# Performance work log

Hardware: AMD Instinct MI355X
Metric: run time of the kernel (lower is better)

## Reference

```python
import jax, jax.numpy as jnp
import numpy as np

WINDOW = 5  # len_sort_window in the original module


def setup_inputs() -> dict:
    key = jax.random.key(0)
    k1, k2, k3 = jax.random.split(key, 3)
    B, L, D = 8, 4000, 512  # L divisible by WINDOW, D < L
    q = jax.random.normal(k1, (B, L, D), dtype=jnp.float32)
    k = jax.random.normal(k2, (B, L, D), dtype=jnp.float32)
    v = jax.random.normal(k3, (B, L, D), dtype=jnp.float32)
    return {"q": q, "k": k, "v": v}


def reference(q, k, v):
    # q, k are unused by the original forward.
    B, L, D = v.shape
    t = jnp.arange(L)          # sequence positions
    s = jnp.arange(D)          # per-feature cyclic shift amount (= feature index)
    # Shift feature i left by i: shifted[:, t, i] = v[:, (t + i) % L, i]
    idx_fwd = (t[:, None] + s[None, :]) % L            # [L, D]
    v_shift = jnp.take_along_axis(v, idx_fwd[None, :, :], axis=1)  # [B, L, D]
    # Sort within fixed non-overlapping windows of size WINDOW along the seq axis.
    v_sorted = jnp.sort(v_shift.reshape(B, L // WINDOW, WINDOW, D), axis=2)
    v_sorted = v_sorted.reshape(B, L, D)
    # Unshift feature i right by i: out[:, t, i] = v_sorted[:, (t - i) % L, i]
    idx_bwd = (t[:, None] - s[None, :]) % L            # [L, D]
    return jnp.take_along_axis(v_sorted, idx_bwd[None, :, :], axis=1)
```

## Files before the change

### kernel.cpp

```cpp
#include <hip/hip_runtime.h>


constexpr int L = 4000;
constexpr int D = 512;

__global__ __launch_bounds__(256)
void swd18_window_sort(const float* __restrict__ v, float* __restrict__ out) {
    const int i = blockIdx.y * 256 + threadIdx.x;
    const int w = blockIdx.x;
    const int b = blockIdx.z;

    const int r = i % 5;
    const int s = w * 5 + r;

    const float* __restrict__ vb = v + (size_t)b * (size_t)(L * D);
    float*       __restrict__ ob = out + (size_t)b * (size_t)(L * D);

    int t0 = s;
    int t1 = s + 1; if (t1 >= L) t1 -= L;
    int t2 = s + 2; if (t2 >= L) t2 -= L;
    int t3 = s + 3; if (t3 >= L) t3 -= L;
    int t4 = s + 4; if (t4 >= L) t4 -= L;

    float x0 = vb[t0 * D + i];
    float x1 = vb[t1 * D + i];
    float x2 = vb[t2 * D + i];
    float x3 = vb[t3 * D + i];
    float x4 = vb[t4 * D + i];

#define CE(a, b) { float lo_ = fminf(a, b); float hi_ = fmaxf(a, b); a = lo_; b = hi_; }
    CE(x0, x1) CE(x3, x4) CE(x2, x4) CE(x2, x3) CE(x1, x4)
    CE(x0, x3) CE(x0, x2) CE(x1, x3) CE(x1, x2)
#undef CE

    ob[t0 * D + i] = x0;
    ob[t1 * D + i] = x1;
    ob[t2 * D + i] = x2;
    ob[t3 * D + i] = x3;
    ob[t4 * D + i] = x4;
}

extern "C" void kernel_launch(void* const* d_in, const int* in_sizes, int n_in,
                              void* d_out, int out_size, void* d_ws, size_t ws_size,
                              hipStream_t stream) {
    const float* v = (const float*)d_in[2];
    float* out = (float*)d_out;

    const int B = in_sizes[2] / (L * D);

    dim3 grid(L / 5, D / 256, B);
    swd18_window_sort<<<grid, dim3(256), 0, stream>>>(v, out);
}
```

Baseline: 193.7 us.

## Stage row tiles with halo in LDS and sort windows from shared memory

Each block now loads a 48-row by 128-column tile (40 output rows plus a 4-row wrap-around halo) into LDS with float4 loads. It runs the 5-element sorting network on every window overlapping that tile, then writes the 40 owned rows back with float4 stores. This replaces per-thread scalar gathers at staggered row offsets with coalesced vector traffic. The cost is about 20% redundant halo reads and two block barriers.

```diff
diff --git a/kernel.cpp b/kernel.cpp
--- a/kernel.cpp
+++ b/kernel.cpp
@@ -3,41 +3,65 @@
 
 constexpr int L = 4000;
 constexpr int D = 512;
+constexpr int TROWS = 40;
+constexpr int RROWS = 48;
+constexpr int CCOLS = 128;
+constexpr int NTHREADS = 256;
 
-__global__ __launch_bounds__(256)
-void swd18_window_sort(const float* __restrict__ v, float* __restrict__ out) {
-    const int i = blockIdx.y * 256 + threadIdx.x;
-    const int w = blockIdx.x;
-    const int b = blockIdx.z;
+__global__ __launch_bounds__(NTHREADS)
+void swd18_tile_sort(const float* __restrict__ v, float* __restrict__ out) {
+    __shared__ float tile[RROWS * CCOLS];
 
-    const int r = i % 5;
-    const int s = w * 5 + r;
+    const int tid = threadIdx.x;
+    const int w   = blockIdx.x;
+    const int C0  = blockIdx.y * CCOLS;
+    const int b   = blockIdx.z;
+    const int R0  = w * TROWS;
 
-    const float* __restrict__ vb = v + (size_t)b * (size_t)(L * D);
-    float*       __restrict__ ob = out + (size_t)b * (size_t)(L * D);
+    const float* __restrict__ vb = v   + (size_t)b * (L * D) + C0;
+    float*       __restrict__ ob = out + (size_t)b * (L * D) + C0;
 
-    int t0 = s;
-    int t1 = s + 1; if (t1 >= L) t1 -= L;
-    int t2 = s + 2; if (t2 >= L) t2 -= L;
-    int t3 = s + 3; if (t3 >= L) t3 -= L;
-    int t4 = s + 4; if (t4 >= L) t4 -= L;
+    for (int idx = tid; idx < RROWS * (CCOLS / 4); idx += NTHREADS) {
+        int lr = idx >> 5;
+        int c4 = (idx & 31) << 2;
+        int g  = R0 - 4 + lr;
+        if (g < 0)  g += L;
+        if (g >= L) g -= L;
+        float4 val = *(const float4*)(vb + (size_t)g * D + c4);
+        *(float4*)(&tile[lr * CCOLS + c4]) = val;
+    }
+    __syncthreads();
 
-    float x0 = vb[t0 * D + i];
-    float x1 = vb[t1 * D + i];
-    float x2 = vb[t2 * D + i];
-    float x3 = vb[t3 * D + i];
-    float x4 = vb[t4 * D + i];
+    for (int id = tid; id < 9 * CCOLS; id += NTHREADS) {
+        int col = id & (CCOLS - 1);
+        int k   = id >> 7;
+        int r   = (C0 + col) % 5;
+        int ls  = r - 1 + 5 * k;
+        if (ls < 0) continue;
+        float* p = &tile[ls * CCOLS + col];
+        float x0 = p[0 * CCOLS];
+        float x1 = p[1 * CCOLS];
+        float x2 = p[2 * CCOLS];
+        float x3 = p[3 * CCOLS];
+        float x4 = p[4 * CCOLS];
+#define CE(a, b) { float lo_ = fminf(a, b); float hi_ = fmaxf(a, b); a = lo_; b = hi_; }
+        CE(x0, x1) CE(x3, x4) CE(x2, x4) CE(x2, x3) CE(x1, x4)
+        CE(x0, x3) CE(x0, x2) CE(x1, x3) CE(x1, x2)
+#undef CE
+        p[0 * CCOLS] = x0;
+        p[1 * CCOLS] = x1;
+        p[2 * CCOLS] = x2;
+        p[3 * CCOLS] = x3;
+        p[4 * CCOLS] = x4;
+    }
+    __syncthreads();
 
-#define CE(a, b) { float lo_ = fminf(a, b); float hi_ = fmaxf(a, b); a = lo_; b = hi_; }
-    CE(x0, x1) CE(x3, x4) CE(x2, x4) CE(x2, x3) CE(x1, x4)
-    CE(x0, x3) CE(x0, x2) CE(x1, x3) CE(x1, x2)
-#undef CE
-
-    ob[t0 * D + i] = x0;
-    ob[t1 * D + i] = x1;
-    ob[t2 * D + i] = x2;
-    ob[t3 * D + i] = x3;
-    ob[t4 * D + i] = x4;
+    for (int idx = tid; idx < TROWS * (CCOLS / 4); idx += NTHREADS) {
+        int lr = (idx >> 5) + 4;
+        int c4 = (idx & 31) << 2;
+        int g  = R0 + lr - 4;
+        *(float4*)(ob + (size_t)g * D + c4) = *(const float4*)(&tile[lr * CCOLS + c4]);
+    }
 }
 
 extern "C" void kernel_launch(void* const* d_in, const int* in_sizes, int n_in,
@@ -48,6 +72,6 @@
 
     const int B = in_sizes[2] / (L * D);
 
-    dim3 grid(L / 5, D / 256, B);
-    swd18_window_sort<<<grid, dim3(256), 0, stream>>>(v, out);
+    dim3 grid(L / TROWS, D / CCOLS, B);
+    swd18_tile_sort<<<grid, dim3(NTHREADS), 0, stream>>>(v, out);
 }
```

Measured after the change: 184.0 us. 1.05x faster.

## Stream row strips per thread with float4 loads and register-carried window state

Applied to the files above, without the earlier changes.

Replaces the one-thread-per-window scalar kernel with threads that each own four adjacent feature columns and walk a 50-row strip. Loads are float4 and are software-pipelined one 5-row group ahead. Each column's shifted sort windows straddle two row groups, so the previous group and the pending output fragments are kept in registers and stitched with selects. The goal is wider memory transactions and less per-thread overhead. The cost is higher register pressure, select-heavy code, and a halo re-read of the previous group at each strip boundary.

```diff
diff --git a/kernel.cpp b/kernel.cpp
--- a/kernel.cpp
+++ b/kernel.cpp
@@ -3,42 +3,95 @@
 
 constexpr int L = 4000;
 constexpr int D = 512;
+constexpr int S = 50;
+constexpr int NSTRIPS = L / S;
+constexpr int NCG = D / 4;
 
-__global__ __launch_bounds__(256)
-void swd18_window_sort(const float* __restrict__ v, float* __restrict__ out) {
-    const int i = blockIdx.y * 256 + threadIdx.x;
-    const int w = blockIdx.x;
-    const int b = blockIdx.z;
+#define CE(a, b) { float lo_ = fminf(a, b); float hi_ = fmaxf(a, b); (a) = lo_; (b) = hi_; }
 
-    const int r = i % 5;
-    const int s = w * 5 + r;
+#define PROC_COL(C, RC)                                                          \
+  {                                                                              \
+    const bool e0 = (RC) == 0, e1 = (RC) == 1, e2 = (RC) == 2, e3 = (RC) == 3;   \
+    float W0 = e0 ? pg[0].C : e1 ? pg[1].C : e2 ? pg[2].C : e3 ? pg[3].C : pg[4].C;  \
+    float W1 = e0 ? pg[1].C : e1 ? pg[2].C : e2 ? pg[3].C : e3 ? pg[4].C : cg_[0].C; \
+    float W2 = e0 ? pg[2].C : e1 ? pg[3].C : e2 ? pg[4].C : e3 ? cg_[0].C : cg_[1].C;\
+    float W3 = e0 ? pg[3].C : e1 ? pg[4].C : e2 ? cg_[0].C : e3 ? cg_[1].C : cg_[2].C;\
+    float W4 = e0 ? pg[4].C : e1 ? cg_[0].C : e2 ? cg_[1].C : e3 ? cg_[2].C : cg_[3].C;\
+    CE(W0, W1) CE(W3, W4) CE(W2, W4) CE(W2, W3) CE(W1, W4)                       \
+    CE(W0, W3) CE(W0, W2) CE(W1, W3) CE(W1, W2)                                  \
+    fa[0].C = e0 ? W0 : ogb[0].C;                                                \
+    fa[1].C = e0 ? W1 : e1 ? W0 : ogb[1].C;                                      \
+    fa[2].C = e0 ? W2 : e1 ? W1 : e2 ? W0 : ogb[2].C;                            \
+    fa[3].C = e0 ? W3 : e1 ? W2 : e2 ? W1 : e3 ? W0 : ogb[3].C;                  \
+    fa[4].C = e0 ? W4 : e1 ? W3 : e2 ? W2 : e3 ? W1 : W0;                        \
+    nb[0].C = e1 ? W4 : e2 ? W3 : e3 ? W2 : W1;              \
+    nb[1].C = e2 ? W4 : e3 ? W3 : W2;                        \
+    nb[2].C = e3 ? W4 : W3;                                  \
+    nb[3].C = W4;                                            \
+    nb[4].C = W4;                                            \
+  }
 
-    const float* __restrict__ vb = v + (size_t)b * (size_t)(L * D);
-    float*       __restrict__ ob = out + (size_t)b * (size_t)(L * D);
+__global__ __launch_bounds__(64)
+void swd18_stream(const float* __restrict__ v, float* __restrict__ out) {
+    const int tid   = blockIdx.x * 64 + threadIdx.x;
+    const int cgidx = tid & (NCG - 1);
+    const int rem   = tid >> 7;
+    const int strip = rem % NSTRIPS;
+    const int b     = rem / NSTRIPS;
 
-    int t0 = s;
-    int t1 = s + 1; if (t1 >= L) t1 -= L;
-    int t2 = s + 2; if (t2 >= L) t2 -= L;
-    int t3 = s + 3; if (t3 >= L) t3 -= L;
-    int t4 = s + 4; if (t4 >= L) t4 -= L;
+    const int R0 = strip * S;
+    const float* __restrict__ vb = v   + (size_t)b * (L * D) + cgidx * 4;
+    float*       __restrict__ ob = out + (size_t)b * (L * D) + cgidx * 4;
 
-    float x0 = vb[t0 * D + i];
-    float x1 = vb[t1 * D + i];
-    float x2 = vb[t2 * D + i];
-    float x3 = vb[t3 * D + i];
-    float x4 = vb[t4 * D + i];
+    const int rc0 = (4 * cgidx) % 5;
+    const int rc1 = (rc0 + 1) % 5;
+    const int rc2 = (rc0 + 2) % 5;
+    const int rc3 = (rc0 + 3) % 5;
 
-#define CE(a, b) { float lo_ = fminf(a, b); float hi_ = fmaxf(a, b); a = lo_; b = hi_; }
-    CE(x0, x1) CE(x3, x4) CE(x2, x4) CE(x2, x3) CE(x1, x4)
-    CE(x0, x3) CE(x0, x2) CE(x1, x3) CE(x1, x2)
+    float4 pg[5], cg_[5], ogb[5];
+
+    int prow = R0 - 5; if (prow < 0) prow += L;
+#pragma unroll
+    for (int j = 0; j < 5; ++j) pg[j]  = *(const float4*)(vb + (size_t)(prow + j) * D);
+#pragma unroll
+    for (int j = 0; j < 5; ++j) cg_[j] = *(const float4*)(vb + (size_t)(R0 + j) * D);
+#pragma unroll
+    for (int j = 0; j < 5; ++j) ogb[j] = make_float4(0.f, 0.f, 0.f, 0.f);
+
+#pragma unroll
+    for (int k = 0; k <= S / 5; ++k) {
+        float4 ng[5];
+        if (k < S / 5) {
+            int nbase = R0 + 5 * (k + 1);
+            if (nbase >= L) nbase -= L;
+#pragma unroll
+            for (int j = 0; j < 5; ++j) ng[j] = *(const float4*)(vb + (size_t)(nbase + j) * D);
+        }
+
+        float4 fa[5], nb[5];
+        PROC_COL(x, rc0)
+        PROC_COL(y, rc1)
+        PROC_COL(z, rc2)
+        PROC_COL(w, rc3)
+
+        if (k > 0) {
+            const int obase = R0 + 5 * k - 5;
+#pragma unroll
+            for (int j = 0; j < 5; ++j)
+                *(float4*)(ob + (size_t)(obase + j) * D) = fa[j];
+        }
+
+#pragma unroll
+        for (int j = 0; j < 5; ++j) {
+            pg[j]  = cg_[j];
+            if (k < S / 5) cg_[j] = ng[j];
+            ogb[j] = nb[j];
+        }
+    }
+}
+
+#undef PROC_COL
 #undef CE
-
-    ob[t0 * D + i] = x0;
-    ob[t1 * D + i] = x1;
-    ob[t2 * D + i] = x2;
-    ob[t3 * D + i] = x3;
-    ob[t4 * D + i] = x4;
-}
 
 extern "C" void kernel_launch(void* const* d_in, const int* in_sizes, int n_in,
                               void* d_out, int out_size, void* d_ws, size_t ws_size,
@@ -47,7 +100,6 @@
     float* out = (float*)d_out;
 
     const int B = in_sizes[2] / (L * D);
-
-    dim3 grid(L / 5, D / 256, B);
-    swd18_window_sort<<<grid, dim3(256), 0, stream>>>(v, out);
+    const int nthreads = NCG * NSTRIPS * B;
+    swd18_stream<<<dim3(nthreads / 64), dim3(64), 0, stream>>>(v, out);
 }
```

Measured after the change: 184.4 us. 4.8% less time.

## Vectorize window sort with output-owned windows and neighbor recompute

Applied to the files above, without the earlier changes.

Reorganizes work so each thread owns one output window of 5 rows across 4 contiguous features. It loads the previous, current and next input windows as float4 and recomputes the two overlapping shifted sorts in registers. Writes use vectorized nontemporal stores. This targets the low-efficiency scalar accesses, at the cost of extra redundant reads and duplicated sorting work.

```diff
diff --git a/kernel.cpp b/kernel.cpp
--- a/kernel.cpp
+++ b/kernel.cpp
@@ -3,42 +3,78 @@
 
 constexpr int L = 4000;
 constexpr int D = 512;
+constexpr int NCG = D / 4;
+constexpr int NG  = L / 5;
+
+typedef float vf4 __attribute__((ext_vector_type(4)));
+
+#define CE(a, b) { float lo_ = fminf(a, b); float hi_ = fmaxf(a, b); (a) = lo_; (b) = hi_; }
+
+#define PROC_COL(C, RC)                                                            \
+  {                                                                                \
+    const bool e0 = (RC) == 0, e1 = (RC) == 1, e2 = (RC) == 2, e3 = (RC) == 3;     \
+    float A0 = e0 ? pg[0][C] : e1 ? pg[1][C] : e2 ? pg[2][C] : e3 ? pg[3][C] : pg[4][C];  \
+    float A1 = e0 ? pg[1][C] : e1 ? pg[2][C] : e2 ? pg[3][C] : e3 ? pg[4][C] : cg_[0][C]; \
+    float A2 = e0 ? pg[2][C] : e1 ? pg[3][C] : e2 ? pg[4][C] : e3 ? cg_[0][C] : cg_[1][C];\
+    float A3 = e0 ? pg[3][C] : e1 ? pg[4][C] : e2 ? cg_[0][C] : e3 ? cg_[1][C] : cg_[2][C];\
+    float A4 = e0 ? pg[4][C] : e1 ? cg_[0][C] : e2 ? cg_[1][C] : e3 ? cg_[2][C] : cg_[3][C];\
+    float B0 = e0 ? cg_[0][C] : e1 ? cg_[1][C] : e2 ? cg_[2][C] : e3 ? cg_[3][C] : cg_[4][C];\
+    float B1 = e0 ? cg_[1][C] : e1 ? cg_[2][C] : e2 ? cg_[3][C] : e3 ? cg_[4][C] : ng[0][C]; \
+    float B2 = e0 ? cg_[2][C] : e1 ? cg_[3][C] : e2 ? cg_[4][C] : e3 ? ng[0][C] : ng[1][C];  \
+    float B3 = e0 ? cg_[3][C] : e1 ? cg_[4][C] : e2 ? ng[0][C] : e3 ? ng[1][C] : ng[2][C];   \
+    float B4 = e0 ? cg_[4][C] : e1 ? ng[0][C] : e2 ? ng[1][C] : e3 ? ng[2][C] : ng[3][C];    \
+    CE(A0, A1) CE(A3, A4) CE(A2, A4) CE(A2, A3) CE(A1, A4)                         \
+    CE(A0, A3) CE(A0, A2) CE(A1, A3) CE(A1, A2)                                    \
+    CE(B0, B1) CE(B3, B4) CE(B2, B4) CE(B2, B3) CE(B1, B4)                         \
+    CE(B0, B3) CE(B0, B2) CE(B1, B3) CE(B1, B2)                                    \
+    fa[0][C] = e0 ? B0 : e1 ? A4 : e2 ? A3 : e3 ? A2 : A1;                         \
+    fa[1][C] = e0 ? B1 : e1 ? B0 : e2 ? A4 : e3 ? A3 : A2;                         \
+    fa[2][C] = e0 ? B2 : e1 ? B1 : e2 ? B0 : e3 ? A4 : A3;                         \
+    fa[3][C] = e0 ? B3 : e1 ? B2 : e2 ? B1 : e3 ? B0 : A4;                         \
+    fa[4][C] = e0 ? B4 : e1 ? B3 : e2 ? B2 : e3 ? B1 : B0;                         \
+  }
 
 __global__ __launch_bounds__(256)
-void swd18_window_sort(const float* __restrict__ v, float* __restrict__ out) {
-    const int i = blockIdx.y * 256 + threadIdx.x;
-    const int w = blockIdx.x;
-    const int b = blockIdx.z;
+void swd18_oneshot(const float* __restrict__ v, float* __restrict__ out) {
+    const int tid = blockIdx.x * 256 + threadIdx.x;
+    const int cg  = tid & (NCG - 1);
+    const int rem = tid >> 7;
+    const int g   = rem % NG;
+    const int b   = rem / NG;
 
-    const int r = i % 5;
-    const int s = w * 5 + r;
+    const float* __restrict__ vb = v   + (size_t)b * (L * D) + cg * 4;
+    float*       __restrict__ ob = out + (size_t)b * (L * D) + cg * 4;
 
-    const float* __restrict__ vb = v + (size_t)b * (size_t)(L * D);
-    float*       __restrict__ ob = out + (size_t)b * (size_t)(L * D);
+    const int r0 = 5 * g;
+    int rp = r0 - 5; if (rp < 0)  rp += L;
+    int rn = r0 + 5; if (rn >= L) rn -= L;
 
-    int t0 = s;
-    int t1 = s + 1; if (t1 >= L) t1 -= L;
-    int t2 = s + 2; if (t2 >= L) t2 -= L;
-    int t3 = s + 3; if (t3 >= L) t3 -= L;
-    int t4 = s + 4; if (t4 >= L) t4 -= L;
+    vf4 pg[5], cg_[5], ng[5];
+#pragma unroll
+    for (int j = 0; j < 5; ++j) pg[j]  = *(const vf4*)(vb + (size_t)(rp + j) * D);
+#pragma unroll
+    for (int j = 0; j < 5; ++j) cg_[j] = *(const vf4*)(vb + (size_t)(r0 + j) * D);
+#pragma unroll
+    for (int j = 0; j < 5; ++j) ng[j]  = *(const vf4*)(vb + (size_t)(rn + j) * D);
 
-    float x0 = vb[t0 * D + i];
-    float x1 = vb[t1 * D + i];
-    float x2 = vb[t2 * D + i];
-    float x3 = vb[t3 * D + i];
-    float x4 = vb[t4 * D + i];
+    const int rc0 = (4 * cg) % 5;
+    const int rc1 = (rc0 + 1) % 5;
+    const int rc2 = (rc0 + 2) % 5;
+    const int rc3 = (rc0 + 3) % 5;
 
-#define CE(a, b) { float lo_ = fminf(a, b); float hi_ = fmaxf(a, b); a = lo_; b = hi_; }
-    CE(x0, x1) CE(x3, x4) CE(x2, x4) CE(x2, x3) CE(x1, x4)
-    CE(x0, x3) CE(x0, x2) CE(x1, x3) CE(x1, x2)
+    vf4 fa[5];
+    PROC_COL(0, rc0)
+    PROC_COL(1, rc1)
+    PROC_COL(2, rc2)
+    PROC_COL(3, rc3)
+
+#pragma unroll
+    for (int j = 0; j < 5; ++j)
+        __builtin_nontemporal_store(fa[j], (vf4*)(ob + (size_t)(r0 + j) * D));
+}
+
+#undef PROC_COL
 #undef CE
-
-    ob[t0 * D + i] = x0;
-    ob[t1 * D + i] = x1;
-    ob[t2 * D + i] = x2;
-    ob[t3 * D + i] = x3;
-    ob[t4 * D + i] = x4;
-}
 
 extern "C" void kernel_launch(void* const* d_in, const int* in_sizes, int n_in,
                               void* d_out, int out_size, void* d_ws, size_t ws_size,
@@ -47,7 +83,6 @@
     float* out = (float*)d_out;
 
     const int B = in_sizes[2] / (L * D);
-
-    dim3 grid(L / 5, D / 256, B);
-    swd18_window_sort<<<grid, dim3(256), 0, stream>>>(v, out);
+    const int nthreads = NCG * NG * B;
+    swd18_oneshot<<<dim3(nthreads / 256), dim3(256), 0, stream>>>(v, out);
 }
```

Result: faster. 178.9 us (-7.6%).
